# Kernel optimization log

Hardware: AMD Instinct MI355X
Metric: run time of the kernel (lower is better)

Reference implementation:

```python
import jax, jax.numpy as jnp
import numpy as np
import math

V, B, C, H, W, D, G, N = 4, 2, 32, 128, 128, 32, 8, 4
ATTN_TEMP = 2.0


def _bilinear_sample(img, gx, gy):
    """img: (C,Hs,Ws); gx,gy: (P,) normalized coords in [-1,1].
    PyTorch grid_sample(mode=bilinear, padding=zeros, align_corners=True)."""
    Cc, Hs, Ws = img.shape
    x = (gx + 1.0) * 0.5 * (Ws - 1)
    y = (gy + 1.0) * 0.5 * (Hs - 1)
    x0 = jnp.floor(x)
    y0 = jnp.floor(y)
    wx = x - x0
    wy = y - y0
    x0i = x0.astype(jnp.int32)
    y0i = y0.astype(jnp.int32)

    def gather(xi, yi):
        valid = ((xi >= 0) & (xi < Ws) & (yi >= 0) & (yi < Hs)).astype(img.dtype)
        v = img[:, jnp.clip(yi, 0, Hs - 1), jnp.clip(xi, 0, Ws - 1)]
        return v * valid

    v00 = gather(x0i, y0i)
    v01 = gather(x0i + 1, y0i)
    v10 = gather(x0i, y0i + 1)
    v11 = gather(x0i + 1, y0i + 1)
    return (v00 * (1 - wx) + v01 * wx) * (1 - wy) + (v10 * (1 - wx) + v11 * wx) * wy


_bilinear_batched = jax.vmap(_bilinear_sample)  # over batch


def _homo_warp(src_fea, src_proj, ref_proj, depth):
    """src_fea (B,C,Hs,Ws), projs (B,4,4), depth (B,D,H,W) -> (B,C,D,H,W)."""
    Bb, Cc, Hs, Ws = src_fea.shape
    Dd, Hr, Wr = depth.shape[1], depth.shape[2], depth.shape[3]
    proj = src_proj @ jnp.linalg.inv(ref_proj)
    rot = proj[:, :3, :3]
    trans = proj[:, :3, 3]  # (B,3)
    yy, xx = jnp.meshgrid(jnp.arange(Hr, dtype=jnp.float32),
                          jnp.arange(Wr, dtype=jnp.float32), indexing='ij')
    xyz = jnp.stack([xx.ravel(), yy.ravel(), jnp.ones(Hr * Wr, jnp.float32)], 0)  # (3,P)
    rot_xyz = jnp.einsum('bij,jp->bip', rot, xyz)  # (B,3,P)
    pts = rot_xyz[:, :, None, :] * depth.reshape(Bb, 1, Dd, Hr * Wr) \
          + trans[:, :, None, None]  # (B,3,D,P)
    z = pts[:, 2]
    z = jnp.where(z == 0.0, 1e-9, z)
    gx = pts[:, 0] / z / ((Ws - 1) / 2.0) - 1.0  # (B,D,P)
    gy = pts[:, 1] / z / ((Hs - 1) / 2.0) - 1.0
    # grid built under torch.no_grad in the original
    gx = jax.lax.stop_gradient(gx).reshape(Bb, Dd * Hr * Wr)
    gy = jax.lax.stop_gradient(gy).reshape(Bb, Dd * Hr * Wr)
    warped = _bilinear_batched(src_fea, gx, gy)  # (B,C,D*P)
    return warped.reshape(Bb, Cc, Dd, Hr, Wr)


def setup_inputs() -> dict:
    key = jax.random.key(0)
    ks = jax.random.split(key, 6)
    ref_features = jax.random.normal(ks[0], (V, B, C, H, W), jnp.float32)
    src_features = jax.random.normal(ks[1], (V, B, C, H, W), jnp.float32)
    # structured camera matrices: [.,.,0]=extrinsic, [.,.,1]=intrinsic
    f = 100.0
    K = np.eye(4, dtype=np.float32)
    K[0, 0] = f; K[1, 1] = f; K[0, 2] = W / 2.0; K[1, 2] = H / 2.0
    projs = np.zeros((B, V + 1, 2, 4, 4), np.float32)
    for v in range(V + 1):
        ang = 0.0 if v == 0 else 0.02 * v
        ca, sa = math.cos(ang), math.sin(ang)
        E = np.eye(4, dtype=np.float32)
        E[:3, :3] = np.array([[ca, 0, sa], [0, 1, 0], [-sa, 0, ca]], np.float32)
        E[0, 3] = 0.0 if v == 0 else 5.0 * v
        projs[:, v, 0] = E
        projs[:, v, 1] = K
    proj_matrices = jnp.asarray(projs)
    dvals = jnp.linspace(425.0, 935.0, D, dtype=jnp.float32)
    depth_hypo = dvals[None, :, None, None] * jnp.ones((B, D, H, W), jnp.float32)
    sample_grids = 2.0 * jax.random.uniform(ks[2], (V, B, N, H, W, 2), jnp.float32) - 1.0
    w_reg = jax.random.normal(ks[3], (G,), jnp.float32) * 0.1
    w_enh = jax.random.normal(ks[4], (G, G * N), jnp.float32) * 0.05
    return {
        'ref_features': ref_features,
        'src_features': src_features,
        'proj_matrices': proj_matrices,
        'depth_hypo': depth_hypo,
        'sample_grids': sample_grids,
        'w_reg': w_reg,
        'w_enh': w_enh,
        'group_cor_dim': G,
        'stage_idx': 3,
    }


def reference(ref_features, src_features, proj_matrices, depth_hypo,
              sample_grids, w_reg, w_enh, group_cor_dim, stage_idx):
    Bb, Dd, Hh, Ww = depth_hypo.shape
    Cc = ref_features.shape[2]
    Gg = group_cor_dim
    ref_proj = proj_matrices[:, 0]
    ref_proj_new = ref_proj[:, 0].at[:, :3, :4].set(
        jnp.einsum('bij,bjk->bik', ref_proj[:, 1, :3, :3], ref_proj[:, 0, :3, :4]))
    cor_weight_sum = 1e-8
    cor_feats = 0.0
    cor_weights = []
    for src_idx in range(V):
        src_proj = proj_matrices[:, src_idx + 1]
        src_proj_new = src_proj[:, 0].at[:, :3, :4].set(
            jnp.einsum('bij,bjk->bik', src_proj[:, 1, :3, :3], src_proj[:, 0, :3, :4]))
        warped_src = _homo_warp(src_features[src_idx], src_proj_new, ref_proj_new,
                                depth_hypo)  # (B,C,D,H,W)
        ref_vol = ref_features[src_idx][:, :, None].reshape(Bb, Gg, Cc // Gg, 1, Hh, Ww)
        wsrc = warped_src.reshape(Bb, Gg, Cc // Gg, Dd, Hh, Ww)
        cor_feat = (wsrc * ref_vol).mean(2)  # (B,G,D,H,W) group correlation
        # --- regcorr: second grid_sample along epipolar-line samples ---
        cf = cor_feat.reshape(Bb, Gg * Dd, Hh, Ww)
        grids = sample_grids[src_idx].reshape(Bb, N * Hh * Ww, 2)
        cf_s = _bilinear_batched(cf, grids[..., 0], grids[..., 1])  # (B,G*D,N*H*W)
        cf_s = cf_s.reshape(Bb, Gg, Dd, N, Hh, Ww)
        cf_s = jnp.transpose(cf_s, (0, 1, 3, 2, 4, 5)).reshape(Bb, Gg * N, Dd, Hh, Ww)
        # line_cross_enhanced_net stand-in: learned mix of line samples, residual add
        cor_feat = cor_feat + jnp.einsum('gk,bkdhw->bgdhw', w_enh, cf_s)
        # --- attn_fuse_d softmax fusion across depth ---
        cor_weight = jax.nn.softmax(cor_feat.sum(1) / ATTN_TEMP, axis=1) / math.sqrt(Cc)
        cor_weight_sum = cor_weight_sum + cor_weight
        cor_weights.append(cor_weight.max(1))
        cor_feats = cor_feats + cor_weight[:, None] * cor_feat
    cor_feats = cor_feats / cor_weight_sum[:, None]
    # regnet stand-in: linear reduction over group dim
    attn_logits = jnp.einsum('g,bgdhw->bdhw', w_reg, cor_feats)
    attn_weight = jax.nn.softmax(attn_logits, axis=1)
    idx = jnp.argmax(attn_weight, axis=1)  # (B,H,W)
    depth = jnp.take_along_axis(depth_hypo, idx[:, None], axis=1)[:, 0]
    # stage_idx=3 -> interpolate scale_factor=1 (identity)
    photometric_confidence = attn_weight.max(1)
    return depth, photometric_confidence, attn_weight, jnp.stack(cor_weights)
```

## Files before the change

### kernel.cpp

```cpp
#include <hip/hip_runtime.h>

#define Vv 4
#define Bn 2
#define Cn 32
#define Hn 128
#define Wn 128
#define Dn 32
#define Gn 8
#define Nn 4
#define HW (Hn*Wn)
#define BHW (Bn*Hn*Wn)
#define DHW (Dn*Hn*Wn)
#define BDHW (Bn*Dn*Hn*Wn)
#define NBLK (DHW/256)
#define RBLK (Gn*HW/256)
#define SBLK (BDHW/256)
#define NST  (Vv*Bn)
#define CAPPX 24

__global__ void setup_proj(const float* __restrict__ pm,
                           const float* __restrict__ wenh,
                           const float* __restrict__ wreg,
                           double* __restrict__ projws,
                           double* __restrict__ wtab) {
    int t = threadIdx.x;
    if (t < Gn) wtab[t] = (double)wreg[t];
    if (t < Gn * Nn) {
        double a = 0.0, c = 0.0;
        for (int g = 0; g < Gn; g++) {
            double wv = (double)wenh[g * (Gn * Nn) + t];
            a += wv;
            c += (double)wreg[g] * wv;
        }
        wtab[8 + t] = a; wtab[40 + t] = c;
    }
    if (t >= Vv * Bn) return;
    int v = t / Bn, b = t % Bn;
    const float* Eref = pm + (((size_t)b * (Vv + 1) + 0) * 2 + 0) * 16;
    const float* Kref = pm + (((size_t)b * (Vv + 1) + 0) * 2 + 1) * 16;
    const float* Esrc = pm + (((size_t)b * (Vv + 1) + (v + 1)) * 2 + 0) * 16;
    const float* Ksrc = pm + (((size_t)b * (Vv + 1) + (v + 1)) * 2 + 1) * 16;
    double R[16], S[16];
    for (int r = 0; r < 3; r++)
        for (int c = 0; c < 4; c++) {
            R[r*4+c] = (double)Kref[r*4+0]*Eref[0*4+c] + (double)Kref[r*4+1]*Eref[1*4+c] + (double)Kref[r*4+2]*Eref[2*4+c];
            S[r*4+c] = (double)Ksrc[r*4+0]*Esrc[0*4+c] + (double)Ksrc[r*4+1]*Esrc[1*4+c] + (double)Ksrc[r*4+2]*Esrc[2*4+c];
        }
    for (int c = 0; c < 4; c++) { R[12+c] = Eref[12+c]; S[12+c] = Esrc[12+c]; }
    double M[4][8];
    for (int r = 0; r < 4; r++)
        for (int c = 0; c < 4; c++) { M[r][c] = R[r*4+c]; M[r][4+c] = (r == c) ? 1.0 : 0.0; }
    for (int col = 0; col < 4; col++) {
        int piv = col; double best = fabs(M[col][col]);
        for (int r = col+1; r < 4; r++) { double a = fabs(M[r][col]); if (a > best) { best = a; piv = r; } }
        if (piv != col)
            for (int c = 0; c < 8; c++) { double tmp = M[col][c]; M[col][c] = M[piv][c]; M[piv][c] = tmp; }
        double inv = 1.0 / M[col][col];
        for (int c = 0; c < 8; c++) M[col][c] *= inv;
        for (int r = 0; r < 4; r++) if (r != col) {
            double f = M[r][col];
            for (int c = 0; c < 8; c++) M[r][c] -= f * M[col][c];
        }
    }
    double P[16];
    for (int r = 0; r < 4; r++)
        for (int c = 0; c < 4; c++) {
            double acc = 0.0;
            for (int k = 0; k < 4; k++) acc += S[r*4+k] * M[k][4+c];
            P[r*4+c] = acc;
        }
    double* o = projws + t * 12;
    o[0]=P[0];  o[1]=P[1];  o[2]=P[2];
    o[3]=P[4];  o[4]=P[5];  o[5]=P[6];
    o[6]=P[8];  o[7]=P[9];  o[8]=P[10];
    o[9]=P[3];  o[10]=P[7]; o[11]=P[11];
}

__device__ __forceinline__ void repack_body(
    int tid, const float* __restrict__ srcf, const float* __restrict__ reff,
    float4* __restrict__ qsrc, float4* __restrict__ qref, int v, int b)
{
    int p = tid & (HW - 1);
    int g = tid >> 14;
    const float* sb = srcf + ((size_t)(v*Bn + b)) * Cn * HW + (size_t)(g*4) * HW + p;
    const float* rb = reff + ((size_t)(v*Bn + b)) * Cn * HW + (size_t)(g*4) * HW + p;
    float4 s4; s4.x = sb[0]; s4.y = sb[HW]; s4.z = sb[2*HW]; s4.w = sb[3*HW];
    float4 r4; r4.x = rb[0]; r4.y = rb[HW]; r4.z = rb[2*HW]; r4.w = rb[3*HW];
    qsrc[(size_t)g * HW + p] = s4;
    qref[(size_t)g * HW + p] = r4;
}

__global__ __launch_bounds__(256) void mega_repack(
    const float* __restrict__ srcf, const float* __restrict__ reff,
    float4* __restrict__ qs_all, float4* __restrict__ qr_all)
{
    int s = blockIdx.x >> 9;
    int tid = (blockIdx.x & 511) * 256 + threadIdx.x;
    int v = s & 3, b = s >> 2;
    repack_body(tid, srcf, reff, qs_all + (size_t)s * Gn * HW,
                qr_all + (size_t)s * Gn * HW, v, b);
}

__global__ __launch_bounds__(256) void mega_warp_lds(
    const float4* __restrict__ qs_all, const float4* __restrict__ qr_all,
    const float* __restrict__ dh, const double* __restrict__ projws,
    const double* __restrict__ wtab,
    float2* __restrict__ own_all, float2* __restrict__ tap_all)
{
    __shared__ float sU1[Gn * Nn], sU2[Gn * Nn], sR[Gn];
    __shared__ float4 span[8][Gn * CAPPX];
    int lt = threadIdx.x;
    if (lt < Gn * Nn) { sU1[lt] = (float)wtab[8 + lt]; sU2[lt] = (float)wtab[40 + lt]; }
    if (lt < Gn) sR[lt] = (float)wtab[lt];
    __syncthreads();

    int s   = blockIdx.x >> 11;
    int bid = blockIdx.x & 2047;
    int v = s & 3, b = s >> 2;
    const float4* qsrc = qs_all + (size_t)s * Gn * HW;
    const float4* qref = qr_all + (size_t)s * Gn * HW;
    float2* ownbuf = own_all + (size_t)s * DHW;
    float2* tapbuf = tap_all + (size_t)s * Nn * DHW;

    int d  = lt & 31;
    int pg = lt >> 5;
    int p  = bid * 8 + pg;
    int w = p & 127, h = p >> 7;
    const double* pr = projws + (v * Bn + b) * 12;
    double xf = (double)w, yf = (double)h;
    double depth = (double)dh[(size_t)(b * Dn + d) * HW + p];
    float px = (float)((pr[0]*xf + pr[1]*yf + pr[2]) * depth + pr[9]);
    float py = (float)((pr[3]*xf + pr[4]*yf + pr[5]) * depth + pr[10]);
    float pz = (float)((pr[6]*xf + pr[7]*yf + pr[8]) * depth + pr[11]);
    if (pz == 0.f) pz = 1e-9f;
    float invz = __frcp_rn(pz);
    float xs = px * invz;
    float ys = py * invz;
    float x0f = floorf(xs), y0f = floorf(ys);
    float wx = xs - x0f, wy = ys - y0f;
    int ix = (int)x0f, iy = (int)y0f;
    bool vx0 = (ix >= 0) && (ix < Wn), vx1 = (ix + 1 >= 0) && (ix + 1 < Wn);
    bool vy0 = (iy >= 0) && (iy < Hn), vy1 = (iy + 1 >= 0) && (iy + 1 < Hn);
    int cx0 = min(max(ix, 0), Wn-1), cx1 = min(max(ix+1, 0), Wn-1);
    int cy0 = min(max(iy, 0), Hn-1), cy1 = min(max(iy+1, 0), Hn-1);
    float a00 = (vx0 && vy0) ? (1.f-wx)*(1.f-wy) : 0.f;
    float a01 = (vx1 && vy0) ? wx*(1.f-wy)       : 0.f;
    float a10 = (vx0 && vy1) ? (1.f-wx)*wy       : 0.f;
    float a11 = (vx1 && vy1) ? wx*wy             : 0.f;

    int xmn = cx0, xmx = cx1, ymn = cy0, ymx = cy1;
    #pragma unroll
    for (int mask = 16; mask >= 1; mask >>= 1) {
        xmn = min(xmn, __shfl_xor(xmn, mask));
        xmx = max(xmx, __shfl_xor(xmx, mask));
        ymn = min(ymn, __shfl_xor(ymn, mask));
        ymx = max(ymx, __shfl_xor(ymx, mask));
    }
    int spanW = xmx - xmn + 1;
    int cnt = spanW * (ymx - ymn + 1);

    float4 rr[Gn];
    #pragma unroll
    for (int j = 0; j < Gn; j++) rr[j] = qref[(size_t)j * HW + p];

    float cor[Gn];
    if (cnt <= CAPPX) {
        if (d < cnt) {
            int sy = ymn + d / spanW;
            int sx = xmn + d % spanW;
            const float4* srcp = qsrc + (size_t)sy * Wn + sx;
            #pragma unroll
            for (int j = 0; j < Gn; j++)
                span[pg][j * CAPPX + d] = srcp[(size_t)j * HW];
        }
        int o00 = (cy0 - ymn) * spanW + (cx0 - xmn);
        int o01 = (cy0 - ymn) * spanW + (cx1 - xmn);
        int o10 = (cy1 - ymn) * spanW + (cx0 - xmn);
        int o11 = (cy1 - ymn) * spanW + (cx1 - xmn);
        #pragma unroll
        for (int j = 0; j < Gn; j++) {
            const float4* sp = &span[pg][j * CAPPX];
            float4 T00 = sp[o00], T01 = sp[o01], T10 = sp[o10], T11 = sp[o11];
            float vx = a00*T00.x + a01*T01.x + a10*T10.x + a11*T11.x;
            float vy = a00*T00.y + a01*T01.y + a10*T10.y + a11*T11.y;
            float vz = a00*T00.z + a01*T01.z + a10*T10.z + a11*T11.z;
            float vw = a00*T00.w + a01*T01.w + a10*T10.w + a11*T11.w;
            cor[j] = ((vx*rr[j].x + vy*rr[j].y) + vz*rr[j].z) + vw*rr[j].w;
        }
    } else {
        int o00 = cy0*Wn + cx0, o01 = cy0*Wn + cx1;
        int o10 = cy1*Wn + cx0, o11 = cy1*Wn + cx1;
        #pragma unroll
        for (int j = 0; j < Gn; j++) {
            const float4* qs = qsrc + (size_t)j * HW;
            float4 T00 = qs[o00], T01 = qs[o01], T10 = qs[o10], T11 = qs[o11];
            float vx = a00*T00.x + a01*T01.x + a10*T10.x + a11*T11.x;
            float vy = a00*T00.y + a01*T01.y + a10*T10.y + a11*T11.y;
            float vz = a00*T00.z + a01*T01.z + a10*T10.z + a11*T11.z;
            float vw = a00*T00.w + a01*T01.w + a10*T10.w + a11*T11.w;
            cor[j] = ((vx*rr[j].x + vy*rr[j].y) + vz*rr[j].z) + vw*rr[j].w;
        }
    }

    float s_own = 0.f, r_own = 0.f;
    #pragma unroll
    for (int g = 0; g < Gn; g++) { s_own += cor[g]; r_own += sR[g] * cor[g]; }
    float2 o2; o2.x = 0.25f * s_own; o2.y = 0.25f * r_own;
    ownbuf[(size_t)p * Dn + d] = o2;
    #pragma unroll
    for (int n = 0; n < Nn; n++) {
        float t1 = 0.f, t2 = 0.f;
        #pragma unroll
        for (int g = 0; g < Gn; g++) {
            t1 += sU1[g*Nn + n] * cor[g];
            t2 += sU2[g*Nn + n] * cor[g];
        }
        float2 t; t.x = 0.25f * t1; t.y = 0.25f * t2;
        tapbuf[((size_t)p * Nn + n) * Dn + d] = t;
    }
}

__device__ __forceinline__ void warp_body(
    int tid, const float* __restrict__ srcf, const float* __restrict__ reff,
    const float* __restrict__ dh, const double* __restrict__ projws,
    const float* sU1, const float* sU2, const float* sR,
    float2* __restrict__ ownbuf, float2* __restrict__ tapbuf, int v, int b)
{
    int d = tid & 31, p = tid >> 5;
    int w = p & 127, h = p >> 7;
    const double* pr = projws + (v * Bn + b) * 12;
    double depth = (double)dh[(size_t)(b * Dn + d) * HW + p];
    double xf = (double)w, yf = (double)h;
    double px = (pr[0]*xf + pr[1]*yf + pr[2]) * depth + pr[9];
    double py = (pr[3]*xf + pr[4]*yf + pr[5]) * depth + pr[10];
    double pz = (pr[6]*xf + pr[7]*yf + pr[8]) * depth + pr[11];
    if (pz == 0.0) pz = 1e-9;
    double invz = 1.0 / pz;
    double xs = px * invz;
    double ys = py * invz;
    double x0f = floor(xs), y0f = floor(ys);
    double wx = xs - x0f, wy = ys - y0f;
    int ix = (int)x0f, iy = (int)y0f;
    bool vx0 = (ix >= 0) && (ix < Wn), vx1 = (ix + 1 >= 0) && (ix + 1 < Wn);
    bool vy0 = (iy >= 0) && (iy < Hn), vy1 = (iy + 1 >= 0) && (iy + 1 < Hn);
    int cx0 = min(max(ix, 0), Wn-1), cx1 = min(max(ix+1, 0), Wn-1);
    int cy0 = min(max(iy, 0), Hn-1), cy1 = min(max(iy+1, 0), Hn-1);
    float a00 = (vx0 && vy0) ? (float)((1.0-wx)*(1.0-wy)) : 0.f;
    float a01 = (vx1 && vy0) ? (float)(wx*(1.0-wy))       : 0.f;
    float a10 = (vx0 && vy1) ? (float)((1.0-wx)*wy)       : 0.f;
    float a11 = (vx1 && vy1) ? (float)(wx*wy)             : 0.f;
    int o00 = cy0*Wn + cx0, o01 = cy0*Wn + cx1, o10 = cy1*Wn + cx0, o11 = cy1*Wn + cx1;
    const float* sb = srcf + ((size_t)(v*Bn + b)) * Cn * HW;
    const float* rb = reff + ((size_t)(v*Bn + b)) * Cn * HW + p;
    float cor[Gn];
    #pragma unroll
    for (int g = 0; g < Gn; g++) cor[g] = 0.f;
    #pragma unroll
    for (int c = 0; c < Cn; c++) {
        const float* sc = sb + c * HW;
        float val = a00*sc[o00] + a01*sc[o01] + a10*sc[o10] + a11*sc[o11];
        cor[c >> 2] += val * rb[c * HW];
    }
    float s_own = 0.f, r_own = 0.f;
    #pragma unroll
    for (int g = 0; g < Gn; g++) { s_own += cor[g]; r_own += sR[g] * cor[g]; }
    float2 o2; o2.x = 0.25f * s_own; o2.y = 0.25f * r_own;
    ownbuf[tid] = o2;
    #pragma unroll
    for (int n = 0; n < Nn; n++) {
        float t1 = 0.f, t2 = 0.f;
        #pragma unroll
        for (int g = 0; g < Gn; g++) {
            t1 += sU1[g*Nn + n] * cor[g];
            t2 += sU2[g*Nn + n] * cor[g];
        }
        float2 t; t.x = 0.25f * t1; t.y = 0.25f * t2;
        tapbuf[((size_t)p * Nn + n) * Dn + d] = t;
    }
}

__device__ __forceinline__ void sample_view(
    int d, int p, int w, int h,
    const float2* __restrict__ ownbuf, const float2* __restrict__ tapbuf,
    const float* __restrict__ grids, float* __restrict__ out_corw,
    int v, int b, double& cw_out, double& r_out)
{
    float2 ow = ownbuf[(size_t)p * Dn + d];
    const float2* gb2 = (const float2*)(grids + ((size_t)(v*Bn + b)) * Nn * HW * 2);
    double A00[Nn], A01[Nn], A10[Nn], A11[Nn];
    int O00[Nn], O01[Nn], O10[Nn], O11[Nn];
    #pragma unroll
    for (int n = 0; n < Nn; n++) {
        float2 g2 = gb2[((size_t)n * Hn + h) * Wn + w];
        double gx = (double)g2.x, gy = (double)g2.y;
        double xs = (gx + 1.0) * 63.5;
        double ys = (gy + 1.0) * 63.5;
        double x0f = floor(xs), y0f = floor(ys);
        double wx = xs - x0f, wy = ys - y0f;
        int ix = (int)x0f, iy = (int)y0f;
        bool vx0 = (ix >= 0) && (ix < Wn), vx1 = (ix + 1 >= 0) && (ix + 1 < Wn);
        bool vy0 = (iy >= 0) && (iy < Hn), vy1 = (iy + 1 >= 0) && (iy + 1 < Hn);
        int cx0 = min(max(ix, 0), Wn-1), cx1 = min(max(ix+1, 0), Wn-1);
        int cy0 = min(max(iy, 0), Hn-1), cy1 = min(max(iy+1, 0), Hn-1);
        A00[n] = (vx0 && vy0) ? (1.0-wx)*(1.0-wy) : 0.0;
        A01[n] = (vx1 && vy0) ? wx*(1.0-wy)       : 0.0;
        A10[n] = (vx0 && vy1) ? (1.0-wx)*wy       : 0.0;
        A11[n] = (vx1 && vy1) ? wx*wy             : 0.0;
        O00[n] = cy0*Wn + cx0; O01[n] = cy0*Wn + cx1;
        O10[n] = cy1*Wn + cx0; O11[n] = cy1*Wn + cx1;
    }
    float2 Q00[Nn], Q01[Nn], Q10[Nn], Q11[Nn];
    #pragma unroll
    for (int n = 0; n < Nn; n++) {
        Q00[n] = tapbuf[((size_t)O00[n] * Nn + n) * Dn + d];
        Q01[n] = tapbuf[((size_t)O01[n] * Nn + n) * Dn + d];
        Q10[n] = tapbuf[((size_t)O10[n] * Nn + n) * Dn + d];
        Q11[n] = tapbuf[((size_t)O11[n] * Nn + n) * Dn + d];
    }
    double s = (double)ow.x, r = (double)ow.y;
    #pragma unroll
    for (int n = 0; n < Nn; n++) {
        s += A00[n]*(double)Q00[n].x + A01[n]*(double)Q01[n].x
           + A10[n]*(double)Q10[n].x + A11[n]*(double)Q11[n].x;
        r += A00[n]*(double)Q00[n].y + A01[n]*(double)Q01[n].y
           + A10[n]*(double)Q10[n].y + A11[n]*(double)Q11[n].y;
    }
    double logit = s * 0.5;
    double m = logit;
    #pragma unroll
    for (int mask = 16; mask >= 1; mask >>= 1) m = fmax(m, __shfl_xor(m, mask));
    double e = exp(logit - m);
    double ssum = e;
    #pragma unroll
    for (int mask = 16; mask >= 1; mask >>= 1) ssum += __shfl_xor(ssum, mask);
    const double SQRTC = 5.656854249492381;
    if (d == 0) out_corw[(size_t)v * BHW + (size_t)b * HW + p] = (float)(1.0 / ssum / SQRTC);
    cw_out = e / ssum / SQRTC;
    r_out = r;
}

__device__ __forceinline__ void finalize_core(
    int d, int p, int b, double cs, double wr,
    const float* __restrict__ depth_hypo, float* __restrict__ out)
{
    double lg = wr / cs;
    double fm = lg;
    #pragma unroll
    for (int mask = 16; mask >= 1; mask >>= 1) fm = fmax(fm, __shfl_xor(fm, mask));
    double fe = exp(lg - fm);
    double fsum = fe;
    #pragma unroll
    for (int mask = 16; mask >= 1; mask >>= 1) fsum += __shfl_xor(fsum, mask);
    out[2*BHW + (size_t)b * DHW + (size_t)d * HW + p] = (float)(fe / fsum);
    double bv = lg; int bi = d;
    #pragma unroll
    for (int mask = 16; mask >= 1; mask >>= 1) {
        double ov = __shfl_xor(bv, mask);
        int oi = __shfl_xor(bi, mask);
        if (ov > bv || (ov == bv && oi < bi)) { bv = ov; bi = oi; }
    }
    double rv = (d == bi) ? -1e300 : lg; int ri = d;
    #pragma unroll
    for (int mask = 16; mask >= 1; mask >>= 1) {
        double ov = __shfl_xor(rv, mask);
        int oi = __shfl_xor(ri, mask);
        if (ov > rv || (ov == rv && oi < ri)) { rv = ov; ri = oi; }
    }
    if (d == 0) {
        const float* dhb = depth_hypo + (size_t)b * DHW + p;
        double eps = 5e-3 * (1.0 + fabs(bv));
        bool adj = (ri == bi + 1) || (ri == bi - 1);
        float dep;
        if (adj && (bv - rv) <= eps)
            dep = 0.5f * (dhb[(size_t)bi * HW] + dhb[(size_t)ri * HW]);
        else
            dep = dhb[(size_t)bi * HW];
        out[(size_t)b * HW + p] = dep;
        out[BHW + (size_t)b * HW + p] = (float)(1.0 / fsum);
    }
}

__global__ __launch_bounds__(256, 3) void mega_sample(
    const float2* __restrict__ own_all, const float2* __restrict__ tap_all,
    const float* __restrict__ grids, const float* __restrict__ dh,
    float* __restrict__ out_corw, float* __restrict__ out)
{
    int tid = blockIdx.x * 256 + threadIdx.x;
    int d = tid & 31;
    int p = (tid >> 5) & (HW - 1);
    int b = tid >> 19;
    int w = p & 127, h = p >> 7;
    double cs = 1e-8, wr = 0.0;
    for (int v = 0; v < Vv; v++) {
        int s = b * 4 + v;
        double cw, r;
        sample_view(d, p, w, h, own_all + (size_t)s * DHW,
                    tap_all + (size_t)s * Nn * DHW, grids, out_corw, v, b, cw, r);
        cs += cw;
        wr += cw * r;
    }
    finalize_core(d, p, b, cs, wr, dh, out);
}

template <int MODE>
__device__ __forceinline__ void sample_body(
    int tid, const float2* __restrict__ ownbuf, const float2* __restrict__ tapbuf,
    const float* __restrict__ grids, float2* __restrict__ accf,
    float* __restrict__ out_corw, const float* __restrict__ depth_hypo,
    float* __restrict__ out, int v, int b)
{
    int d = tid & 31;
    int p = tid >> 5;
    int w = p & 127, h = p >> 7;
    double cw, r;
    sample_view(d, p, w, h, ownbuf, tapbuf, grids, out_corw, v, b, cw, r);
    if (MODE == 0) {
        float2 a; a.x = (float)(1e-8 + cw); a.y = (float)(cw * r);
        accf[tid] = a;
    } else if (MODE == 1) {
        float2 a = accf[tid];
        a.x = (float)((double)a.x + cw);
        a.y = (float)((double)a.y + cw * r);
        accf[tid] = a;
    } else {
        float2 a = accf[tid];
        finalize_core(d, p, b, (double)a.x + cw, (double)a.y + cw * r, depth_hypo, out);
    }
}

__global__ __launch_bounds__(256) void warp_corr(
    const float* __restrict__ srcf, const float* __restrict__ reff,
    const float* __restrict__ dh, const double* __restrict__ projws,
    const double* __restrict__ wtab,
    float2* __restrict__ ownbuf, float2* __restrict__ tapbuf, int v, int b)
{
    __shared__ float sU1[Gn * Nn], sU2[Gn * Nn], sR[Gn];
    int lt = threadIdx.x;
    if (lt < Gn * Nn) { sU1[lt] = (float)wtab[8 + lt]; sU2[lt] = (float)wtab[40 + lt]; }
    if (lt < Gn) sR[lt] = (float)wtab[lt];
    __syncthreads();
    warp_body(blockIdx.x * 256 + lt, srcf, reff, dh, projws, sU1, sU2, sR,
              ownbuf, tapbuf, v, b);
}

template <int MODE>
__global__ __launch_bounds__(256) void sample_enh(
    const float2* __restrict__ ownbuf, const float2* __restrict__ tapbuf,
    const float* __restrict__ grids, float2* __restrict__ accf,
    float* __restrict__ out_corw, const float* __restrict__ depth_hypo,
    float* __restrict__ out, int v, int b)
{
    sample_body<MODE>(blockIdx.x * 256 + threadIdx.x, ownbuf, tapbuf, grids,
                      accf, out_corw, depth_hypo, out, v, b);
}

template <int MODE>
__global__ __launch_bounds__(256) void fused_sw(
    const float* __restrict__ srcf, const float* __restrict__ reff,
    const float* __restrict__ dh, const double* __restrict__ projws,
    const double* __restrict__ wtab, const float* __restrict__ grids,
    const float2* __restrict__ ownR, const float2* __restrict__ tapR,
    float2* __restrict__ ownW, float2* __restrict__ tapW,
    float2* __restrict__ accf, float* __restrict__ out_corw,
    float* __restrict__ out, int vs, int bs, int vw, int bw)
{
    int lt = threadIdx.x;
    int role = blockIdx.x & 1;
    int vb   = blockIdx.x >> 1;
    if (role == 0) {
        sample_body<MODE>(vb * 256 + lt, ownR, tapR, grids,
                          accf, out_corw, dh, out, vs, bs);
    } else {
        __shared__ float sU1[Gn * Nn], sU2[Gn * Nn], sR[Gn];
        if (lt < Gn * Nn) { sU1[lt] = (float)wtab[8 + lt]; sU2[lt] = (float)wtab[40 + lt]; }
        if (lt < Gn) sR[lt] = (float)wtab[lt];
        __syncthreads();
        warp_body(vb * 256 + lt, srcf, reff, dh, projws,
                  sU1, sU2, sR, ownW, tapW, vw, bw);
    }
}

extern "C" void kernel_launch(void* const* d_in, const int* in_sizes, int n_in,
                              void* d_out, int out_size, void* d_ws, size_t ws_size,
                              hipStream_t stream) {
    const float* reff  = (const float*)d_in[0];
    const float* srcf  = (const float*)d_in[1];
    const float* pm    = (const float*)d_in[2];
    const float* dh    = (const float*)d_in[3];
    const float* grids = (const float*)d_in[4];
    const float* wreg  = (const float*)d_in[5];
    const float* wenh  = (const float*)d_in[6];
    float* out = (float*)d_out;
    double* projws = (double*)d_ws;
    double* wtab   = (double*)((char*)d_ws + 1024);
    char*   base   = (char*)d_ws + 2048;
    float2* tap_all = (float2*)base;
    float2* own_all = tap_all + (size_t)NST * Nn * DHW;
    float4* qs_all  = (float4*)(own_all + (size_t)NST * DHW);
    float4* qr_all  = qs_all + (size_t)NST * Gn * HW;
    size_t need_mega = 2048 + (size_t)NST * Nn * DHW * 8 + (size_t)NST * DHW * 8
                     + 2 * (size_t)NST * Gn * HW * 16;
    float2* accf = (float2*)base;
    float2* own0 = accf + DHW;
    float2* tap0 = own0 + DHW;
    float2* own1 = tap0 + (size_t)DHW * Nn;
    float2* tap1 = own1 + DHW;
    size_t need_pipe = 2048 + (size_t)DHW * 8 + 2 * ((size_t)DHW * 8 + (size_t)DHW * Nn * 8);

    setup_proj<<<1, 64, 0, stream>>>(pm, wenh, wreg, projws, wtab);
    float* out_corw = out + 2*BHW + BDHW;

    if (ws_size >= need_mega) {
        mega_repack<<<NST * RBLK, 256, 0, stream>>>(srcf, reff, qs_all, qr_all);
        mega_warp_lds<<<NST * NBLK, 256, 0, stream>>>(qs_all, qr_all, dh, projws,
                                                      wtab, own_all, tap_all);
        mega_sample<<<SBLK, 256, 0, stream>>>(own_all, tap_all, grids, dh,
                                              out_corw, out);
    } else if (ws_size >= need_pipe) {
        float2* owns[2] = { own0, own1 };
        float2* taps[2] = { tap0, tap1 };
        warp_corr<<<NBLK, 256, 0, stream>>>(srcf, reff, dh, projws, wtab,
                                            own0, tap0, 0, 0);
        for (int k = 1; k < 8; k++) {
            int vs = (k - 1) & 3, bs = (k - 1) >> 2;
            int vw = k & 3,       bw = k >> 2;
            float2* oR = owns[(k - 1) & 1]; float2* tR = taps[(k - 1) & 1];
            float2* oW = owns[k & 1];       float2* tW = taps[k & 1];
            if (vs == 0)
                fused_sw<0><<<2*NBLK, 256, 0, stream>>>(srcf, reff, dh, projws, wtab, grids,
                                                        oR, tR, oW, tW, accf,
                                                        out_corw, out, vs, bs, vw, bw);
            else if (vs == 3)
                fused_sw<2><<<2*NBLK, 256, 0, stream>>>(srcf, reff, dh, projws, wtab, grids,
                                                        oR, tR, oW, tW, accf,
                                                        out_corw, out, vs, bs, vw, bw);
            else
                fused_sw<1><<<2*NBLK, 256, 0, stream>>>(srcf, reff, dh, projws, wtab, grids,
                                                        oR, tR, oW, tW, accf,
                                                        out_corw, out, vs, bs, vw, bw);
        }
        sample_enh<2><<<NBLK, 256, 0, stream>>>(owns[1], taps[1], grids, accf,
                                                out_corw, dh, out, 3, 1);
    } else {
        for (int b = 0; b < Bn; b++) {
            for (int v = 0; v < Vv; v++) {
                warp_corr<<<NBLK, 256, 0, stream>>>(srcf, reff, dh, projws, wtab,
                                                    own0, tap0, v, b);
                if (v == 0)
                    sample_enh<0><<<NBLK, 256, 0, stream>>>(own0, tap0, grids, accf,
                                                            out_corw, dh, out, v, b);
                else if (v < Vv - 1)
                    sample_enh<1><<<NBLK, 256, 0, stream>>>(own0, tap0, grids, accf,
                                                            out_corw, dh, out, v, b);
                else
                    sample_enh<2><<<NBLK, 256, 0, stream>>>(own0, tap0, grids, accf,
                                                            out_corw, dh, out, v, b);
            }
        }
    }
}
```

Baseline: 190.7 us.

## Transpose depth hypotheses to pixel-major and swizzle block order for XCD locality

Adds a small LDS-tiled transpose kernel that converts depth_hypo from (B,D,HW) to (B,HW,D) layout so that the warp kernel, where lanes index depth, reads depth values coalesced instead of with stride HW. It also remaps block indices in mega_warp_lds and mega_sample with a modulo-8 swizzle, so consecutive blocks dispatched round-robin across the chip's 8 XCDs work on contiguous data and share L2. The cost is an extra kernel launch, extra workspace, and a slightly larger workspace threshold for the mega path.

```diff
diff --git a/kernel.cpp b/kernel.cpp
--- a/kernel.cpp
+++ b/kernel.cpp
@@ -76,6 +76,24 @@
     o[9]=P[3];  o[10]=P[7]; o[11]=P[11];
 }
 
+__global__ __launch_bounds__(256) void transpose_depth(
+    const float* __restrict__ in, float* __restrict__ outT)
+{
+    __shared__ float tile[32][33];
+    int b = blockIdx.y;
+    int tx = threadIdx.x, ty = threadIdx.y;
+    int p0 = blockIdx.x * 32;
+    const float* ib = in + (size_t)b * DHW;
+    float* ob = outT + (size_t)b * DHW;
+    #pragma unroll
+    for (int r = ty; r < 32; r += 8)
+        tile[tx][r] = ib[(size_t)r * HW + p0 + tx];
+    __syncthreads();
+    #pragma unroll
+    for (int r = ty; r < 32; r += 8)
+        ob[(size_t)(p0 + r) * 32 + tx] = tile[r][tx];
+}
+
 __device__ __forceinline__ void repack_body(
     int tid, const float* __restrict__ srcf, const float* __restrict__ reff,
     float4* __restrict__ qsrc, float4* __restrict__ qref, int v, int b)
@@ -103,7 +121,7 @@
 
 __global__ __launch_bounds__(256) void mega_warp_lds(
     const float4* __restrict__ qs_all, const float4* __restrict__ qr_all,
-    const float* __restrict__ dh, const double* __restrict__ projws,
+    const float* __restrict__ dhT, const double* __restrict__ projws,
     const double* __restrict__ wtab,
     float2* __restrict__ own_all, float2* __restrict__ tap_all)
 {
@@ -114,8 +132,9 @@
     if (lt < Gn) sR[lt] = (float)wtab[lt];
     __syncthreads();
 
-    int s   = blockIdx.x >> 11;
-    int bid = blockIdx.x & 2047;
+    int swz = (blockIdx.x & 7) * (NST * NBLK / 8) + (blockIdx.x >> 3);
+    int s   = swz >> 11;
+    int bid = swz & 2047;
     int v = s & 3, b = s >> 2;
     const float4* qsrc = qs_all + (size_t)s * Gn * HW;
     const float4* qref = qr_all + (size_t)s * Gn * HW;
@@ -128,7 +147,7 @@
     int w = p & 127, h = p >> 7;
     const double* pr = projws + (v * Bn + b) * 12;
     double xf = (double)w, yf = (double)h;
-    double depth = (double)dh[(size_t)(b * Dn + d) * HW + p];
+    double depth = (double)dhT[(size_t)b * DHW + (size_t)p * Dn + d];
     float px = (float)((pr[0]*xf + pr[1]*yf + pr[2]) * depth + pr[9]);
     float py = (float)((pr[3]*xf + pr[4]*yf + pr[5]) * depth + pr[10]);
     float pz = (float)((pr[6]*xf + pr[7]*yf + pr[8]) * depth + pr[11]);
@@ -385,7 +404,8 @@
     const float* __restrict__ grids, const float* __restrict__ dh,
     float* __restrict__ out_corw, float* __restrict__ out)
 {
-    int tid = blockIdx.x * 256 + threadIdx.x;
+    int vb = (blockIdx.x & 7) * (SBLK / 8) + (blockIdx.x >> 3);
+    int tid = vb * 256 + threadIdx.x;
     int d = tid & 31;
     int p = (tid >> 5) & (HW - 1);
     int b = tid >> 19;
@@ -498,8 +518,9 @@
     float2* own_all = tap_all + (size_t)NST * Nn * DHW;
     float4* qs_all  = (float4*)(own_all + (size_t)NST * DHW);
     float4* qr_all  = qs_all + (size_t)NST * Gn * HW;
+    float*  dhT     = (float*)(qr_all + (size_t)NST * Gn * HW);
     size_t need_mega = 2048 + (size_t)NST * Nn * DHW * 8 + (size_t)NST * DHW * 8
-                     + 2 * (size_t)NST * Gn * HW * 16;
+                     + 2 * (size_t)NST * Gn * HW * 16 + (size_t)BDHW * 4;
     float2* accf = (float2*)base;
     float2* own0 = accf + DHW;
     float2* tap0 = own0 + DHW;
@@ -511,8 +532,9 @@
     float* out_corw = out + 2*BHW + BDHW;
 
     if (ws_size >= need_mega) {
+        transpose_depth<<<dim3(HW/32, Bn), dim3(32, 8), 0, stream>>>(dh, dhT);
         mega_repack<<<NST * RBLK, 256, 0, stream>>>(srcf, reff, qs_all, qr_all);
-        mega_warp_lds<<<NST * NBLK, 256, 0, stream>>>(qs_all, qr_all, dh, projws,
+        mega_warp_lds<<<NST * NBLK, 256, 0, stream>>>(qs_all, qr_all, dhT, projws,
                                                       wtab, own_all, tap_all);
         mega_sample<<<SBLK, 256, 0, stream>>>(own_all, tap_all, grids, dh,
                                               out_corw, out);
```

Measured after the change: 190.1 us. Within noise of the previous version (-0.3%).
